# Kernel optimization log

Hardware: AMD Instinct MI355X
Metric: run time of the kernel (lower is better)

The kernel has to match this reference:

```python
import jax, jax.numpy as jnp
import numpy as np

B, T, D, E, H = 4, 2048, 1024, 4, 8
EPS = 1e-5


def _uniform(k, shape, bound):
    return jax.random.uniform(k, shape, jnp.float32, -bound, bound)


def setup_inputs() -> dict:
    key = jax.random.key(0)
    ks = jax.random.split(key, 12)
    wb = np.sqrt(6.0 / D) / np.sqrt(6.0)  # kaiming_uniform(a=sqrt5) bound ~ 1/sqrt(D)... keep simple
    wb = 1.0 / np.sqrt(D)
    return {
        "x": jax.random.normal(ks[0], (B, T, D), jnp.float32),
        "router_prob": jax.random.uniform(ks[1], (B, T, E), jnp.float32),
        "norm_w": jnp.ones((D,), jnp.float32),
        "norm_b": jnp.zeros((D,), jnp.float32),
        "q_w": _uniform(ks[2], (D, D), wb),
        "q_b": _uniform(ks[3], (D,), wb),
        "k_w": _uniform(ks[4], (D, D), wb),
        "k_b": _uniform(ks[5], (D,), wb),
        "v_w": _uniform(ks[6], (D, D), wb),
        "v_b": _uniform(ks[7], (D,), wb),
        "o_w": _uniform(ks[8], (D, D), wb),
        "o_b": _uniform(ks[9], (D,), wb),
    }


def _layernorm(x, w, b):
    mu = jnp.mean(x, axis=-1, keepdims=True)
    var = jnp.mean(jnp.square(x - mu), axis=-1, keepdims=True)
    return (x - mu) * jax.lax.rsqrt(var + EPS) * w + b


def reference(x, router_prob, norm_w, norm_b, q_w, q_b, k_w, k_b, v_w, v_b, o_w, o_b):
    e_cnt = router_prob.shape[2]
    b, t, d = x.shape
    n = t // e_cnt
    h = H
    scale = d ** (-0.5)  # note: original uses model_dim**-0.5, not head_dim

    qs, ks_, vs = [], [], []
    for e in range(e_cnt):
        xe = x[:, e * n:(e + 1) * n, :]
        xn = _layernorm(xe, norm_w, norm_b)
        m = d // (2 ** e)
        xm = xn[..., :m]  # [b, n, m] matryoshka slice
        # F.linear(xm, W[:, :m], bias): out = xm @ W[:, :m]^T + b -> [b, n, d]
        qs.append(jnp.einsum('bnm,dm->bnd', xm, q_w[:, :m]) + q_b)
        ks_.append(jnp.einsum('bnm,dm->bnd', xm, k_w[:, :m]) + k_b)
        vs.append(jnp.einsum('bnm,dm->bnd', xm, v_w[:, :m]) + v_b)
    q = jnp.concatenate(qs, axis=1)
    k = jnp.concatenate(ks_, axis=1)
    v = jnp.concatenate(vs, axis=1)

    dh = d // h
    q = q.reshape(b, t, h, dh).transpose(0, 2, 1, 3)  # b h t dh
    k = k.reshape(b, t, h, dh).transpose(0, 2, 1, 3)
    v = v.reshape(b, t, h, dh).transpose(0, 2, 1, 3)

    attn = jnp.einsum('bhqd,bhkd->bhqk', q, k) * scale
    attn = jax.nn.softmax(attn, axis=-1)  # dropout = identity in eval
    attn_out = jnp.einsum('bhqk,bhkd->bhqd', attn, v)
    attn_out = attn_out.transpose(0, 2, 1, 3).reshape(b, t, d)

    outs = []
    for e in range(e_cnt):
        sl = slice(e * n, (e + 1) * n)
        m = d // (2 ** e)
        xm = attn_out[:, sl, :m]
        out = jnp.einsum('bnm,om->bno', xm, o_w[:m, :m]) + o_b[:m]  # [b, n, m]
        pad = d - m
        if pad:
            out = jnp.pad(out, ((0, 0), (0, 0), (0, pad)))
        outs.append(out + x[:, sl, :])
    return jnp.concatenate(outs, axis=1)
```

## Files before the change

kernel.cpp:

```cpp
#include <hip/hip_runtime.h>
#include <hip/hip_bf16.h>

#define DEV static __device__ __forceinline__

typedef __attribute__((ext_vector_type(4))) float f32x4;
typedef __attribute__((ext_vector_type(8))) short s16x8;

constexpr int Bn = 4, Tn = 2048, Dn = 1024, Hn = 8, DH = 128;
constexpr float EPSF = 1e-5f;
constexpr float QSCALE = 0.0450842200277801f;

DEV unsigned short f2bf(float f) {
    unsigned int u = __float_as_uint(f);
    u += 0x7FFF + ((u >> 16) & 1);
    return (unsigned short)(u >> 16);
}

DEV f32x4 mfma16(s16x8 a, s16x8 b, f32x4 c) {
    return __builtin_amdgcn_mfma_f32_16x16x32_bf16(a, b, c, 0, 0, 0);
}

DEV float ex2(float x) {
    float r;
    asm("v_exp_f32 %0, %1" : "=v"(r) : "v"(x));
    return r;
}

DEV unsigned int cvtpk(float lo, float hi) {
    unsigned int r;
    asm("v_cvt_pk_bf16_f32 %0, %1, %2" : "=v"(r) : "v"(lo), "v"(hi));
    return r;
}

typedef __attribute__((address_space(1))) const unsigned int GU32;
typedef __attribute__((address_space(3))) unsigned int LU32;
DEV void gload16(const void* g, void* l) {
    __builtin_amdgcn_global_load_lds((GU32*)g, (LU32*)l, 16, 0, 0);
}

__global__ void cvt_w_kernel(const float* __restrict__ qw, const float* __restrict__ kw,
                             const float* __restrict__ vw, const float* __restrict__ ow,
                             unsigned short* __restrict__ dst) {
    int idx = blockIdx.x * blockDim.x + threadIdx.x;
    const int total = 4 * Dn * Dn;
    for (; idx < total; idx += gridDim.x * blockDim.x) {
        int sel = idx >> 20;
        int off = idx & (Dn * Dn - 1);
        const float* src = sel == 0 ? qw : sel == 1 ? kw : sel == 2 ? vw : ow;
        dst[idx] = f2bf(src[off]);
    }
}

__global__ __launch_bounds__(256) void ln_kernel(const float* __restrict__ x,
                                                 const float* __restrict__ w,
                                                 const float* __restrict__ b,
                                                 unsigned short* __restrict__ xn) {
    int tok = blockIdx.x;
    int tid = threadIdx.x;
    const float* xp = x + (size_t)tok * Dn;
    float4 v = ((const float4*)xp)[tid];
    float s = v.x + v.y + v.z + v.w;
    float q = v.x * v.x + v.y * v.y + v.z * v.z + v.w * v.w;
    for (int off = 32; off; off >>= 1) {
        s += __shfl_xor(s, off);
        q += __shfl_xor(q, off);
    }
    __shared__ float red[8];
    __shared__ float stats[2];
    int wid = tid >> 6, lane = tid & 63;
    if (lane == 0) { red[wid] = s; red[4 + wid] = q; }
    __syncthreads();
    if (tid == 0) {
        float ts = red[0] + red[1] + red[2] + red[3];
        float tq = red[4] + red[5] + red[6] + red[7];
        float mu = ts / Dn;
        float var = tq / Dn - mu * mu;
        stats[0] = mu;
        stats[1] = rsqrtf(var + EPSF);
    }
    __syncthreads();
    float mu = stats[0], rs = stats[1];
    int c = tid * 4;
    ushort4 o;
    o.x = f2bf((v.x - mu) * rs * w[c + 0] + b[c + 0]);
    o.y = f2bf((v.y - mu) * rs * w[c + 1] + b[c + 1]);
    o.z = f2bf((v.z - mu) * rs * w[c + 2] + b[c + 2]);
    o.w = f2bf((v.w - mu) * rs * w[c + 3] + b[c + 3]);
    ((ushort4*)(xn + (size_t)tok * Dn))[tid] = o;
}

__global__ __launch_bounds__(256) void qkv_gemm(const unsigned short* __restrict__ xn,
                                                const unsigned short* __restrict__ wmat,
                                                const float* __restrict__ qb_,
                                                const float* __restrict__ kb_,
                                                const float* __restrict__ vb_,
                                                unsigned short* __restrict__ outq,
                                                unsigned short* __restrict__ outk,
                                                unsigned short* __restrict__ vt) {
    int rowbase = blockIdx.x * 128;
    int colbase = blockIdx.y * 128;
    int matid = blockIdx.z;
    const unsigned short* W = wmat + (size_t)matid * Dn * Dn;
    const float* bias = matid == 0 ? qb_ : matid == 1 ? kb_ : vb_;
    float oscale = matid == 0 ? QSCALE : 1.0f;
    int e = (rowbase & (Tn - 1)) >> 9;
    int m = Dn >> e;

    __shared__ alignas(16) unsigned short At[128 * 32];
    __shared__ alignas(16) unsigned short Bt[128 * 32];

    int tid = threadIdx.x;
    int lane = tid & 63, wv = tid >> 6;
    int wr = (wv >> 1) * 64, wc = (wv & 1) * 64;
    int fr = lane & 15, fg = lane >> 4;
    int srow = tid >> 2, scol = (tid & 3) * 8;
    const unsigned short* ga0 = xn + (size_t)(rowbase + srow) * Dn + scol;
    const unsigned short* ga1 = xn + (size_t)(rowbase + 64 + srow) * Dn + scol;
    const unsigned short* gb0 = W + (size_t)(colbase + srow) * Dn + scol;
    const unsigned short* gb1 = W + (size_t)(colbase + 64 + srow) * Dn + scol;
    unsigned short* la0 = At + tid * 8;
    unsigned short* la1 = At + 2048 + tid * 8;
    unsigned short* lb0 = Bt + tid * 8;
    unsigned short* lb1 = Bt + 2048 + tid * 8;

    f32x4 acc[4][4] = {};

    for (int k = 0; k < m; k += 32) {
        __syncthreads();
        gload16(ga0 + k, la0);
        gload16(ga1 + k, la1);
        gload16(gb0 + k, lb0);
        gload16(gb1 + k, lb1);
        __syncthreads();
        s16x8 a[4], b[4];
        #pragma unroll
        for (int i = 0; i < 4; i++) a[i] = *(const s16x8*)&At[(wr + i * 16 + fr) * 32 + fg * 8];
        #pragma unroll
        for (int j = 0; j < 4; j++) b[j] = *(const s16x8*)&Bt[(wc + j * 16 + fr) * 32 + fg * 8];
        #pragma unroll
        for (int i = 0; i < 4; i++)
            #pragma unroll
            for (int j = 0; j < 4; j++) acc[i][j] = mfma16(a[i], b[j], acc[i][j]);
    }

    if (matid == 2) {
        #pragma unroll
        for (int i = 0; i < 4; i++)
            #pragma unroll
            for (int j = 0; j < 4; j++) {
                int col = colbase + wc + j * 16 + fr;
                float bv = bias[col];
                int row0 = rowbase + wr + i * 16 + fg * 4;
                int bb = row0 >> 11, tl = row0 & (Tn - 1);
                size_t base = (((size_t)bb * Hn + (col >> 7)) * DH + (col & (DH - 1))) * Tn + tl;
                ushort4 o;
                o.x = f2bf(acc[i][j][0] + bv);
                o.y = f2bf(acc[i][j][1] + bv);
                o.z = f2bf(acc[i][j][2] + bv);
                o.w = f2bf(acc[i][j][3] + bv);
                *(ushort4*)&vt[base] = o;
            }
    } else {
        unsigned short* out = matid == 0 ? outq : outk;
        #pragma unroll
        for (int i = 0; i < 4; i++)
            #pragma unroll
            for (int j = 0; j < 4; j++) {
                int col = colbase + wc + j * 16 + fr;
                float bv = bias[col];
                #pragma unroll
                for (int r = 0; r < 4; r++) {
                    int row = rowbase + wr + i * 16 + fg * 4 + r;
                    out[(size_t)row * Dn + col] = f2bf((acc[i][j][r] + bv) * oscale);
                }
            }
    }
}

__global__ __launch_bounds__(512, 1) void attn_kernel(const unsigned short* __restrict__ Q,
                                                      const unsigned short* __restrict__ K,
                                                      const unsigned short* __restrict__ VT,
                                                      unsigned short* __restrict__ AO) {
    int b = blockIdx.z, h = blockIdx.y;
    int qbase = blockIdx.x * 256;
    int tid = threadIdx.x;
    int wv = tid >> 6, lane = tid & 63;
    int fr = lane & 15, fg = lane >> 4;

    __shared__ alignas(16) unsigned short Kt[2][64 * 128];
    __shared__ alignas(16) unsigned short Vt[2][128 * 64];
    __shared__ alignas(16) unsigned short Pt[8][32][72];

    s16x8 bq[2][4];
    #pragma unroll
    for (int hh = 0; hh < 2; hh++) {
        const size_t qr = ((size_t)b * Tn + qbase + wv * 32 + hh * 16 + fr) * Dn + h * DH;
        #pragma unroll
        for (int c = 0; c < 4; c++) bq[hh][c] = *(const s16x8*)&Q[qr + c * 32 + fg * 8];
    }

    f32x4 acc[2][8] = {};
    float m_run[2] = {-1e30f, -1e30f};
    float l_run[2] = {0.f, 0.f};

    const unsigned short* Kbase = K + (size_t)b * Tn * Dn + h * DH;
    const unsigned short* Vbase = VT + ((size_t)b * Hn + h) * DH * Tn;

    int krow_lo = tid >> 4, kchk = tid & 15;
    int vrow_lo = tid >> 3, vchk = tid & 7;

    auto STAGE = [&](int t, int buf) {
        int kb = t * 64;
        #pragma unroll
        for (int p = 0; p < 2; p++) {
            int row = p * 32 + krow_lo;
            int chunk = kchk ^ (row & 7);
            gload16(Kbase + (size_t)(kb + row) * Dn + chunk * 8,
                    &Kt[buf][p * 4096 + tid * 8]);
        }
        #pragma unroll
        for (int p = 0; p < 2; p++) {
            int row = p * 64 + vrow_lo;
            int chunk = vchk ^ (row & 7);
            gload16(Vbase + (size_t)row * Tn + kb + chunk * 8,
                    &Vt[buf][p * 4096 + tid * 8]);
        }
    };

    STAGE(0, 0);
    __syncthreads();

    for (int t = 0; t < Tn / 64; t++) {
        int cur = t & 1;
        if (t < Tn / 64 - 1) STAGE(t + 1, cur ^ 1);

        const unsigned short* KtC = &Kt[cur][0];
        const unsigned short* VtC = &Vt[cur][0];

        f32x4 s[2][4] = {};
        #pragma unroll
        for (int c = 0; c < 4; c++) {
            #pragma unroll
            for (int kt = 0; kt < 4; kt++) {
                s16x8 ak = *(const s16x8*)&KtC[(kt * 16 + fr) * 128 +
                                               (((c * 4 + fg) ^ (fr & 7)) * 8)];
                s[0][kt] = mfma16(ak, bq[0][c], s[0][kt]);
                s[1][kt] = mfma16(ak, bq[1][c], s[1][kt]);
            }
        }

        float mx[2];
        #pragma unroll
        for (int hh = 0; hh < 2; hh++) {
            float v = s[hh][0][0];
            #pragma unroll
            for (int kt = 0; kt < 4; kt++)
                #pragma unroll
                for (int r = 0; r < 4; r++) v = fmaxf(v, s[hh][kt][r]);
            v = fmaxf(v, __shfl_xor(v, 16));
            v = fmaxf(v, __shfl_xor(v, 32));
            mx[hh] = v;
        }

        if (!__all(mx[0] - m_run[0] <= 8.0f && mx[1] - m_run[1] <= 8.0f)) {
            #pragma unroll
            for (int hh = 0; hh < 2; hh++) {
                float mnew = fmaxf(m_run[hh], mx[hh]);
                float f = ex2(m_run[hh] - mnew);
                l_run[hh] *= f;
                float fw[4];
                #pragma unroll
                for (int r = 0; r < 4; r++) fw[r] = __shfl(f, fg * 4 + r);
                #pragma unroll
                for (int n = 0; n < 8; n++)
                    #pragma unroll
                    for (int r = 0; r < 4; r++) acc[hh][n][r] *= fw[r];
                m_run[hh] = mnew;
            }
        }

        #pragma unroll
        for (int hh = 0; hh < 2; hh++) {
            float p[16];
            float sum = 0.f;
            #pragma unroll
            for (int kt = 0; kt < 4; kt++)
                #pragma unroll
                for (int r = 0; r < 4; r++) {
                    float ev = ex2(s[hh][kt][r] - m_run[hh]);
                    p[kt * 4 + r] = ev;
                    sum += ev;
                }
            sum += __shfl_xor(sum, 16);
            sum += __shfl_xor(sum, 32);
            l_run[hh] += sum;
            #pragma unroll
            for (int kt = 0; kt < 4; kt++) {
                uint2 w;
                w.x = cvtpk(p[kt * 4 + 0], p[kt * 4 + 1]);
                w.y = cvtpk(p[kt * 4 + 2], p[kt * 4 + 3]);
                *(uint2*)&Pt[wv][hh * 16 + fr][kt * 16 + fg * 4] = w;
            }
        }

        #pragma unroll
        for (int ks = 0; ks < 2; ks++) {
            s16x8 pa0 = *(const s16x8*)&Pt[wv][fr][ks * 32 + fg * 8];
            s16x8 pa1 = *(const s16x8*)&Pt[wv][16 + fr][ks * 32 + fg * 8];
            #pragma unroll
            for (int n = 0; n < 8; n++) {
                s16x8 bv = *(const s16x8*)&VtC[(n * 16 + fr) * 64 +
                                               (((ks * 4 + fg) ^ (fr & 7)) * 8)];
                acc[0][n] = mfma16(pa0, bv, acc[0][n]);
                acc[1][n] = mfma16(pa1, bv, acc[1][n]);
            }
        }
        __syncthreads();
    }

    #pragma unroll
    for (int hh = 0; hh < 2; hh++) {
        float rl[4];
        #pragma unroll
        for (int r = 0; r < 4; r++) rl[r] = 1.0f / __shfl(l_run[hh], fg * 4 + r);
        size_t orow0 = ((size_t)b * Tn + qbase + wv * 32 + hh * 16) * Dn + h * DH;
        for (int n = 0; n < 8; n++)
            for (int r = 0; r < 4; r++) {
                float v = acc[hh][n][r] * rl[r];
                AO[orow0 + (size_t)(fg * 4 + r) * Dn + n * 16 + fr] = f2bf(v);
            }
    }
}

__global__ __launch_bounds__(256) void oproj_gemm(const unsigned short* __restrict__ A,
                                                  const unsigned short* __restrict__ W,
                                                  const float* __restrict__ bias,
                                                  const float* __restrict__ x,
                                                  float* __restrict__ out) {
    int rowbase = blockIdx.x * 128;
    int colbase = blockIdx.y * 128;
    int e = (rowbase & (Tn - 1)) >> 9;
    int m = Dn >> e;
    int tid = threadIdx.x;

    if (colbase >= m) {
        #pragma unroll
        for (int i = 0; i < 16; i++) {
            int idx = i * 256 + tid;
            int r = idx >> 5, c4 = (idx & 31) * 4;
            size_t g = (size_t)(rowbase + r) * Dn + colbase + c4;
            *(float4*)&out[g] = *(const float4*)&x[g];
        }
        return;
    }

    __shared__ alignas(16) unsigned short At[128 * 32];
    __shared__ alignas(16) unsigned short Bt[128 * 32];
    int lane = tid & 63, wv = tid >> 6;
    int wr = (wv >> 1) * 64, wc = (wv & 1) * 64;
    int fr = lane & 15, fg = lane >> 4;
    int srow = tid >> 2, scol = (tid & 3) * 8;
    const unsigned short* ga0 = A + (size_t)(rowbase + srow) * Dn + scol;
    const unsigned short* ga1 = A + (size_t)(rowbase + 64 + srow) * Dn + scol;
    const unsigned short* gb0 = W + (size_t)(colbase + srow) * Dn + scol;
    const unsigned short* gb1 = W + (size_t)(colbase + 64 + srow) * Dn + scol;
    unsigned short* la0 = At + tid * 8;
    unsigned short* la1 = At + 2048 + tid * 8;
    unsigned short* lb0 = Bt + tid * 8;
    unsigned short* lb1 = Bt + 2048 + tid * 8;

    f32x4 acc[4][4] = {};

    for (int k = 0; k < m; k += 32) {
        __syncthreads();
        gload16(ga0 + k, la0);
        gload16(ga1 + k, la1);
        gload16(gb0 + k, lb0);
        gload16(gb1 + k, lb1);
        __syncthreads();
        s16x8 a[4], b[4];
        #pragma unroll
        for (int i = 0; i < 4; i++) a[i] = *(const s16x8*)&At[(wr + i * 16 + fr) * 32 + fg * 8];
        #pragma unroll
        for (int j = 0; j < 4; j++) b[j] = *(const s16x8*)&Bt[(wc + j * 16 + fr) * 32 + fg * 8];
        #pragma unroll
        for (int i = 0; i < 4; i++)
            #pragma unroll
            for (int j = 0; j < 4; j++) acc[i][j] = mfma16(a[i], b[j], acc[i][j]);
    }

    #pragma unroll
    for (int i = 0; i < 4; i++)
        #pragma unroll
        for (int j = 0; j < 4; j++) {
            int col = colbase + wc + j * 16 + fr;
            float bv = bias[col];
            #pragma unroll
            for (int r = 0; r < 4; r++) {
                int row = rowbase + wr + i * 16 + fg * 4 + r;
                size_t g = (size_t)row * Dn + col;
                out[g] = acc[i][j][r] + bv + x[g];
            }
        }
}

extern "C" void kernel_launch(void* const* d_in, const int* in_sizes, int n_in,
                              void* d_out, int out_size, void* d_ws, size_t ws_size,
                              hipStream_t stream) {
    const float* x   = (const float*)d_in[0];
    const float* nw  = (const float*)d_in[2];
    const float* nb  = (const float*)d_in[3];
    const float* qw  = (const float*)d_in[4];
    const float* qb_ = (const float*)d_in[5];
    const float* kw  = (const float*)d_in[6];
    const float* kb_ = (const float*)d_in[7];
    const float* vw  = (const float*)d_in[8];
    const float* vb_ = (const float*)d_in[9];
    const float* ow  = (const float*)d_in[10];
    const float* ob_ = (const float*)d_in[11];
    float* out = (float*)d_out;

    unsigned short* ws = (unsigned short*)d_ws;
    const size_t NTOK = (size_t)Bn * Tn;
    unsigned short* xn = ws;
    unsigned short* qd = xn + NTOK * Dn;
    unsigned short* kd = qd + NTOK * Dn;
    unsigned short* vt = kd + NTOK * Dn;
    unsigned short* ao = vt + NTOK * Dn;
    unsigned short* wb = ao + NTOK * Dn;

    hipLaunchKernelGGL(cvt_w_kernel, dim3(4096), dim3(256), 0, stream, qw, kw, vw, ow, wb);
    hipLaunchKernelGGL(ln_kernel, dim3(NTOK), dim3(256), 0, stream, x, nw, nb, xn);
    hipLaunchKernelGGL(qkv_gemm, dim3(64, 8, 3), dim3(256), 0, stream,
                       xn, wb, qb_, kb_, vb_, qd, kd, vt);
    hipLaunchKernelGGL(attn_kernel, dim3(Tn / 256, Hn, Bn), dim3(512), 0, stream, qd, kd, vt, ao);
    hipLaunchKernelGGL(oproj_gemm, dim3(64, 8), dim3(256), 0, stream,
                       ao, wb + (size_t)3 * Dn * Dn, ob_, x, out);
}
```

Measured before the change: 210.4 us.

## Double-buffer GEMM tiles and retile attention with register-resident P

Both GEMM kernels now use double-buffered shared-memory tiles, so the next K-slice loads while MFMAs run on the current one, with one barrier per iteration instead of two. The attention kernel shrinks to 256-thread blocks over 128 queries with 32-key tiles and a flattened 512-block grid. The softmax probabilities are packed directly into MFMA A-operand registers, which removes the shared-memory P round trip. The cost is more loop iterations and barriers in attention, and split 8-byte V reads with a new swizzle.

Result: slower. 306.8 us (+45.8%).

```diff
diff --git a/kernel.cpp b/kernel.cpp
--- a/kernel.cpp
+++ b/kernel.cpp
@@ -5,6 +5,7 @@
 
 typedef __attribute__((ext_vector_type(4))) float f32x4;
 typedef __attribute__((ext_vector_type(8))) short s16x8;
+typedef __attribute__((ext_vector_type(4))) unsigned int u32x4;
 
 constexpr int Bn = 4, Tn = 2048, Dn = 1024, Hn = 8, DH = 128;
 constexpr float EPSF = 1e-5f;
@@ -106,8 +107,8 @@
     int e = (rowbase & (Tn - 1)) >> 9;
     int m = Dn >> e;
 
-    __shared__ alignas(16) unsigned short At[128 * 32];
-    __shared__ alignas(16) unsigned short Bt[128 * 32];
+    __shared__ alignas(16) unsigned short At[2][128 * 32];
+    __shared__ alignas(16) unsigned short Bt[2][128 * 32];
 
     int tid = threadIdx.x;
     int lane = tid & 63, wv = tid >> 6;
@@ -118,29 +119,34 @@
     const unsigned short* ga1 = xn + (size_t)(rowbase + 64 + srow) * Dn + scol;
     const unsigned short* gb0 = W + (size_t)(colbase + srow) * Dn + scol;
     const unsigned short* gb1 = W + (size_t)(colbase + 64 + srow) * Dn + scol;
-    unsigned short* la0 = At + tid * 8;
-    unsigned short* la1 = At + 2048 + tid * 8;
-    unsigned short* lb0 = Bt + tid * 8;
-    unsigned short* lb1 = Bt + 2048 + tid * 8;
 
     f32x4 acc[4][4] = {};
 
+    gload16(ga0, &At[0][tid * 8]);
+    gload16(ga1, &At[0][2048 + tid * 8]);
+    gload16(gb0, &Bt[0][tid * 8]);
+    gload16(gb1, &Bt[0][2048 + tid * 8]);
+    __syncthreads();
+
     for (int k = 0; k < m; k += 32) {
+        int cur = (k >> 5) & 1;
+        if (k + 32 < m) {
+            int nb = cur ^ 1, kn = k + 32;
+            gload16(ga0 + kn, &At[nb][tid * 8]);
+            gload16(ga1 + kn, &At[nb][2048 + tid * 8]);
+            gload16(gb0 + kn, &Bt[nb][tid * 8]);
+            gload16(gb1 + kn, &Bt[nb][2048 + tid * 8]);
+        }
+        s16x8 a[4], b[4];
+        #pragma unroll
+        for (int i = 0; i < 4; i++) a[i] = *(const s16x8*)&At[cur][(wr + i * 16 + fr) * 32 + fg * 8];
+        #pragma unroll
+        for (int j = 0; j < 4; j++) b[j] = *(const s16x8*)&Bt[cur][(wc + j * 16 + fr) * 32 + fg * 8];
+        #pragma unroll
+        for (int i = 0; i < 4; i++)
+            #pragma unroll
+            for (int j = 0; j < 4; j++) acc[i][j] = mfma16(a[i], b[j], acc[i][j]);
         __syncthreads();
-        gload16(ga0 + k, la0);
-        gload16(ga1 + k, la1);
-        gload16(gb0 + k, lb0);
-        gload16(gb1 + k, lb1);
-        __syncthreads();
-        s16x8 a[4], b[4];
-        #pragma unroll
-        for (int i = 0; i < 4; i++) a[i] = *(const s16x8*)&At[(wr + i * 16 + fr) * 32 + fg * 8];
-        #pragma unroll
-        for (int j = 0; j < 4; j++) b[j] = *(const s16x8*)&Bt[(wc + j * 16 + fr) * 32 + fg * 8];
-        #pragma unroll
-        for (int i = 0; i < 4; i++)
-            #pragma unroll
-            for (int j = 0; j < 4; j++) acc[i][j] = mfma16(a[i], b[j], acc[i][j]);
     }
 
     if (matid == 2) {
@@ -177,19 +183,21 @@
     }
 }
 
-__global__ __launch_bounds__(512, 1) void attn_kernel(const unsigned short* __restrict__ Q,
+__global__ __launch_bounds__(256, 4) void attn_kernel(const unsigned short* __restrict__ Q,
                                                       const unsigned short* __restrict__ K,
                                                       const unsigned short* __restrict__ VT,
                                                       unsigned short* __restrict__ AO) {
-    int b = blockIdx.z, h = blockIdx.y;
-    int qbase = blockIdx.x * 256;
+    int f = blockIdx.x;
+    int qi = f >> 5;
+    int bh = f & 31;
+    int b = bh >> 3, h = bh & 7;
+    int qbase = qi * 128;
     int tid = threadIdx.x;
     int wv = tid >> 6, lane = tid & 63;
     int fr = lane & 15, fg = lane >> 4;
 
-    __shared__ alignas(16) unsigned short Kt[2][64 * 128];
-    __shared__ alignas(16) unsigned short Vt[2][128 * 64];
-    __shared__ alignas(16) unsigned short Pt[8][32][72];
+    __shared__ alignas(16) unsigned short Kt[2][32 * 128];
+    __shared__ alignas(16) unsigned short Vt[2][128 * 32];
 
     s16x8 bq[2][4];
     #pragma unroll
@@ -206,42 +214,42 @@
     const unsigned short* Kbase = K + (size_t)b * Tn * Dn + h * DH;
     const unsigned short* Vbase = VT + ((size_t)b * Hn + h) * DH * Tn;
 
-    int krow_lo = tid >> 4, kchk = tid & 15;
-    int vrow_lo = tid >> 3, vchk = tid & 7;
+    int k_row_lo = tid >> 4, k_chk = tid & 15;
+    int v_row_lo = tid >> 2, v_chk = tid & 3;
 
     auto STAGE = [&](int t, int buf) {
-        int kb = t * 64;
+        int kb = t * 32;
         #pragma unroll
         for (int p = 0; p < 2; p++) {
-            int row = p * 32 + krow_lo;
-            int chunk = kchk ^ (row & 7);
+            int row = p * 16 + k_row_lo;
+            int chunk = k_chk ^ (row & 7);
             gload16(Kbase + (size_t)(kb + row) * Dn + chunk * 8,
-                    &Kt[buf][p * 4096 + tid * 8]);
+                    &Kt[buf][p * 2048 + tid * 8]);
         }
         #pragma unroll
         for (int p = 0; p < 2; p++) {
-            int row = p * 64 + vrow_lo;
-            int chunk = vchk ^ (row & 7);
+            int row = p * 64 + v_row_lo;
+            int chunk = v_chk ^ (row & 3);
             gload16(Vbase + (size_t)row * Tn + kb + chunk * 8,
-                    &Vt[buf][p * 4096 + tid * 8]);
+                    &Vt[buf][p * 2048 + tid * 8]);
         }
     };
 
     STAGE(0, 0);
     __syncthreads();
 
-    for (int t = 0; t < Tn / 64; t++) {
+    for (int t = 0; t < Tn / 32; t++) {
         int cur = t & 1;
-        if (t < Tn / 64 - 1) STAGE(t + 1, cur ^ 1);
+        if (t < Tn / 32 - 1) STAGE(t + 1, cur ^ 1);
 
         const unsigned short* KtC = &Kt[cur][0];
         const unsigned short* VtC = &Vt[cur][0];
 
-        f32x4 s[2][4] = {};
+        f32x4 s[2][2] = {};
         #pragma unroll
         for (int c = 0; c < 4; c++) {
             #pragma unroll
-            for (int kt = 0; kt < 4; kt++) {
+            for (int kt = 0; kt < 2; kt++) {
                 s16x8 ak = *(const s16x8*)&KtC[(kt * 16 + fr) * 128 +
                                                (((c * 4 + fg) ^ (fr & 7)) * 8)];
                 s[0][kt] = mfma16(ak, bq[0][c], s[0][kt]);
@@ -252,11 +260,8 @@
         float mx[2];
         #pragma unroll
         for (int hh = 0; hh < 2; hh++) {
-            float v = s[hh][0][0];
-            #pragma unroll
-            for (int kt = 0; kt < 4; kt++)
-                #pragma unroll
-                for (int r = 0; r < 4; r++) v = fmaxf(v, s[hh][kt][r]);
+            float v = fmaxf(fmaxf(s[hh][0][0], s[hh][0][1]), fmaxf(s[hh][0][2], s[hh][0][3]));
+            v = fmaxf(v, fmaxf(fmaxf(s[hh][1][0], s[hh][1][1]), fmaxf(s[hh][1][2], s[hh][1][3])));
             v = fmaxf(v, __shfl_xor(v, 16));
             v = fmaxf(v, __shfl_xor(v, 32));
             mx[hh] = v;
@@ -266,11 +271,11 @@
             #pragma unroll
             for (int hh = 0; hh < 2; hh++) {
                 float mnew = fmaxf(m_run[hh], mx[hh]);
-                float f = ex2(m_run[hh] - mnew);
-                l_run[hh] *= f;
+                float fsc = ex2(m_run[hh] - mnew);
+                l_run[hh] *= fsc;
                 float fw[4];
                 #pragma unroll
-                for (int r = 0; r < 4; r++) fw[r] = __shfl(f, fg * 4 + r);
+                for (int r = 0; r < 4; r++) fw[r] = __shfl(fsc, fg * 4 + r);
                 #pragma unroll
                 for (int n = 0; n < 8; n++)
                     #pragma unroll
@@ -279,12 +284,13 @@
             }
         }
 
+        s16x8 pa[2];
         #pragma unroll
         for (int hh = 0; hh < 2; hh++) {
-            float p[16];
+            float p[8];
             float sum = 0.f;
             #pragma unroll
-            for (int kt = 0; kt < 4; kt++)
+            for (int kt = 0; kt < 2; kt++)
                 #pragma unroll
                 for (int r = 0; r < 4; r++) {
                     float ev = ex2(s[hh][kt][r] - m_run[hh]);
@@ -294,26 +300,27 @@
             sum += __shfl_xor(sum, 16);
             sum += __shfl_xor(sum, 32);
             l_run[hh] += sum;
-            #pragma unroll
-            for (int kt = 0; kt < 4; kt++) {
-                uint2 w;
-                w.x = cvtpk(p[kt * 4 + 0], p[kt * 4 + 1]);
-                w.y = cvtpk(p[kt * 4 + 2], p[kt * 4 + 3]);
-                *(uint2*)&Pt[wv][hh * 16 + fr][kt * 16 + fg * 4] = w;
-            }
-        }
-
-        #pragma unroll
-        for (int ks = 0; ks < 2; ks++) {
-            s16x8 pa0 = *(const s16x8*)&Pt[wv][fr][ks * 32 + fg * 8];
-            s16x8 pa1 = *(const s16x8*)&Pt[wv][16 + fr][ks * 32 + fg * 8];
-            #pragma unroll
-            for (int n = 0; n < 8; n++) {
-                s16x8 bv = *(const s16x8*)&VtC[(n * 16 + fr) * 64 +
-                                               (((ks * 4 + fg) ^ (fr & 7)) * 8)];
-                acc[0][n] = mfma16(pa0, bv, acc[0][n]);
-                acc[1][n] = mfma16(pa1, bv, acc[1][n]);
-            }
+            u32x4 pw;
+            pw.x = cvtpk(p[0], p[1]);
+            pw.y = cvtpk(p[2], p[3]);
+            pw.z = cvtpk(p[4], p[5]);
+            pw.w = cvtpk(p[6], p[7]);
+            pa[hh] = __builtin_bit_cast(s16x8, pw);
+        }
+
+        #pragma unroll
+        for (int n = 0; n < 8; n++) {
+            int row = n * 16 + fr;
+            const char* vr = (const char*)&VtC[row * 32];
+            int c1 = (fg >> 1) ^ (row & 3);
+            int c2 = (2 + (fg >> 1)) ^ (row & 3);
+            uint2 lo = *(const uint2*)(vr + c1 * 16 + (fg & 1) * 8);
+            uint2 hi = *(const uint2*)(vr + c2 * 16 + (fg & 1) * 8);
+            u32x4 bw;
+            bw.x = lo.x; bw.y = lo.y; bw.z = hi.x; bw.w = hi.y;
+            s16x8 bv = __builtin_bit_cast(s16x8, bw);
+            acc[0][n] = mfma16(pa[0], bv, acc[0][n]);
+            acc[1][n] = mfma16(pa[1], bv, acc[1][n]);
         }
         __syncthreads();
     }
@@ -354,8 +361,8 @@
         return;
     }
 
-    __shared__ alignas(16) unsigned short At[128 * 32];
-    __shared__ alignas(16) unsigned short Bt[128 * 32];
+    __shared__ alignas(16) unsigned short At[2][128 * 32];
+    __shared__ alignas(16) unsigned short Bt[2][128 * 32];
     int lane = tid & 63, wv = tid >> 6;
     int wr = (wv >> 1) * 64, wc = (wv & 1) * 64;
     int fr = lane & 15, fg = lane >> 4;
@@ -364,29 +371,34 @@
     const unsigned short* ga1 = A + (size_t)(rowbase + 64 + srow) * Dn + scol;
     const unsigned short* gb0 = W + (size_t)(colbase + srow) * Dn + scol;
     const unsigned short* gb1 = W + (size_t)(colbase + 64 + srow) * Dn + scol;
-    unsigned short* la0 = At + tid * 8;
-    unsigned short* la1 = At + 2048 + tid * 8;
-    unsigned short* lb0 = Bt + tid * 8;
-    unsigned short* lb1 = Bt + 2048 + tid * 8;
 
     f32x4 acc[4][4] = {};
 
+    gload16(ga0, &At[0][tid * 8]);
+    gload16(ga1, &At[0][2048 + tid * 8]);
+    gload16(gb0, &Bt[0][tid * 8]);
+    gload16(gb1, &Bt[0][2048 + tid * 8]);
+    __syncthreads();
+
     for (int k = 0; k < m; k += 32) {
+        int cur = (k >> 5) & 1;
+        if (k + 32 < m) {
+            int nb = cur ^ 1, kn = k + 32;
+            gload16(ga0 + kn, &At[nb][tid * 8]);
+            gload16(ga1 + kn, &At[nb][2048 + tid * 8]);
+            gload16(gb0 + kn, &Bt[nb][tid * 8]);
+            gload16(gb1 + kn, &Bt[nb][2048 + tid * 8]);
+        }
+        s16x8 a[4], b[4];
+        #pragma unroll
+        for (int i = 0; i < 4; i++) a[i] = *(const s16x8*)&At[cur][(wr + i * 16 + fr) * 32 + fg * 8];
+        #pragma unroll
+        for (int j = 0; j < 4; j++) b[j] = *(const s16x8*)&Bt[cur][(wc + j * 16 + fr) * 32 + fg * 8];
+        #pragma unroll
+        for (int i = 0; i < 4; i++)
+            #pragma unroll
+            for (int j = 0; j < 4; j++) acc[i][j] = mfma16(a[i], b[j], acc[i][j]);
         __syncthreads();
-        gload16(ga0 + k, la0);
-        gload16(ga1 + k, la1);
-        gload16(gb0 + k, lb0);
-        gload16(gb1 + k, lb1);
-        __syncthreads();
-        s16x8 a[4], b[4];
-        #pragma unroll
-        for (int i = 0; i < 4; i++) a[i] = *(const s16x8*)&At[(wr + i * 16 + fr) * 32 + fg * 8];
-        #pragma unroll
-        for (int j = 0; j < 4; j++) b[j] = *(const s16x8*)&Bt[(wc + j * 16 + fr) * 32 + fg * 8];
-        #pragma unroll
-        for (int i = 0; i < 4; i++)
-            #pragma unroll
-            for (int j = 0; j < 4; j++) acc[i][j] = mfma16(a[i], b[j], acc[i][j]);
     }
 
     #pragma unroll
@@ -433,7 +445,7 @@
     hipLaunchKernelGGL(ln_kernel, dim3(NTOK), dim3(256), 0, stream, x, nw, nb, xn);
     hipLaunchKernelGGL(qkv_gemm, dim3(64, 8, 3), dim3(256), 0, stream,
                        xn, wb, qb_, kb_, vb_, qd, kd, vt);
-    hipLaunchKernelGGL(attn_kernel, dim3(Tn / 256, Hn, Bn), dim3(512), 0, stream, qd, kd, vt, ao);
+    hipLaunchKernelGGL(attn_kernel, dim3(512), dim3(256), 0, stream, qd, kd, vt, ao);
     hipLaunchKernelGGL(oproj_gemm, dim3(64, 8), dim3(256), 0, stream,
                        ao, wb + (size_t)3 * Dn * Dn, ob_, x, out);
 }
```
